# Performance work log

Measured on AMD Instinct MI355X. Metric: run time of the kernel, lower is better.

The kernel has to match this reference:

```python
import jax, jax.numpy as jnp
import numpy as np

N_NODES = 10000
N_EDGES = 50000
UNITS = 64
NUM_GAUSSIANS = 50
MIN_D, MAX_D, GAMMA = 0.0, 30.0, 10.0


def setup_inputs() -> dict:
    key = jax.random.key(0)
    ks = jax.random.split(key, 8)
    node_features = jax.random.normal(ks[0], (N_NODES, UNITS), dtype=jnp.float32)
    edge_indices = jax.random.randint(ks[1], (2, N_EDGES), 0, N_NODES, dtype=jnp.int32)
    distances = jax.random.uniform(ks[2], (N_EDGES,), dtype=jnp.float32) * MAX_D
    # filter network params (Dense(units) -> Dense(units*units)), glorot-ish scales
    W1 = jax.random.normal(ks[3], (NUM_GAUSSIANS, UNITS), dtype=jnp.float32) * 0.13
    b1 = jnp.zeros((UNITS,), dtype=jnp.float32)
    W2 = jax.random.normal(ks[4], (UNITS, UNITS * UNITS), dtype=jnp.float32) * 0.02
    b2 = jnp.zeros((UNITS * UNITS,), dtype=jnp.float32)
    # transform Dense(units, use_bias=False)
    Wt = jax.random.normal(ks[5], (UNITS, UNITS), dtype=jnp.float32) * 0.125
    return {"node_features": node_features, "edge_indices": edge_indices,
            "distances": distances, "W1": W1, "b1": b1, "W2": W2, "b2": b2, "Wt": Wt}


def reference(node_features, edge_indices, distances, W1, b1, W2, b2, Wt):
    # Gaussian basis expansion: [E, G]
    centers = jnp.linspace(MIN_D, MAX_D, NUM_GAUSSIANS, dtype=jnp.float32)
    dist_feat = jnp.exp(-GAMMA * jnp.square(distances[:, None] - centers[None, :]))
    # filter-generating network -> per-edge [E, U, U] filters
    h = dist_feat @ W1 + b1
    filters = (h @ W2 + b2).reshape(-1, UNITS, UNITS)
    # gather source node feats, linear transform, per-edge matvec
    src = node_features[edge_indices[0]]            # [E, U]
    transformed = src @ Wt                          # [E, U]
    filtered = jnp.einsum('eij,ej->ei', filters, transformed)  # [E, U]
    # scatter-sum to destination nodes
    messages = jax.ops.segment_sum(filtered, edge_indices[1], num_segments=N_NODES)
    # shifted softplus: f(0) = 0
    return jax.nn.softplus(messages) - jnp.log(jnp.float32(2.0))
```

## Files before the change

kernel.cpp:

```cpp
#include <hip/hip_runtime.h>
#include <stdint.h>

#define UNITS 64
#define UU 4096
#define NG 50
#define NSLOT 51
#define GAMMA_C 10.0f
#define STEP_C (30.0f / 49.0f)
#define NWIN 4
#define NBKT 47
#define NCHK 64

typedef __attribute__((ext_vector_type(8))) short bf16x8;
typedef __attribute__((ext_vector_type(4))) float f32x4;

union bfr_t { bf16x8 v; uint32_t u[4]; };

__device__ __forceinline__ uint16_t f2bf(float x) {
  uint32_t u = __float_as_uint(x);
  u += 0x7fffu + ((u >> 16) & 1u);
  return (uint16_t)(u >> 16);
}
__device__ __forceinline__ uint32_t pk_bf16(float lo, float hi) {
  uint32_t r;
  asm("v_cvt_pk_bf16_f32 %0, %1, %2" : "=v"(r) : "v"(lo), "v"(hi));
  return r;
}
__device__ __forceinline__ int lo_of(float d) {
  int lo = (int)floorf(d * (1.0f / STEP_C)) - 1;
  return min(max(lo, 0), NG - NWIN);
}

__global__ void __launch_bounds__(256) k_hist(const float* __restrict__ dist,
                                              int* __restrict__ binsB,
                                              int* __restrict__ eidx, int E, int ne) {
  __shared__ int hloc[NBKT];
  for (int i = threadIdx.x; i < NBKT; i += 256) hloc[i] = 0;
  __syncthreads();
  int per = (E + NCHK - 1) / NCHK;
  int e0 = blockIdx.x * per, e1 = min(e0 + per, E);
  for (int e = e0 + threadIdx.x; e < e1; e += 256)
    atomicAdd(&hloc[lo_of(dist[e])], 1);
  __syncthreads();
  for (int i = threadIdx.x; i < 64; i += 256)
    binsB[blockIdx.x * 64 + i] = (i < NBKT) ? hloc[i] : 0;
  for (int i = blockIdx.x * 256 + threadIdx.x; i < ne; i += NCHK * 256) eidx[i] = -1;
}

__global__ void __launch_bounds__(256) k_at(
    const float* __restrict__ W1, const float* __restrict__ b1,
    const float* __restrict__ W2, const float* __restrict__ b2,
    const float* __restrict__ Wt, const float* __restrict__ dist,
    uint16_t* __restrict__ T5B, float* __restrict__ msg,
    const int* __restrict__ binsB, int* __restrict__ eidx,
    int n_out, int E) {
  int g = blockIdx.y, bx = blockIdx.x;
  if (g >= NSLOT) {
    if (g < NSLOT + 8) {
      int n4 = n_out >> 2;
      float4 z = {0.f, 0.f, 0.f, 0.f};
      for (int t = ((g - NSLOT) * 16 + bx) * 256 + threadIdx.x; t < n4; t += 128 * 256)
        reinterpret_cast<float4*>(msg)[t] = z;
      return;
    }
    __shared__ int hbase[NBKT], hcur[NBKT];
    int sb = (g - (NSLOT + 8)) * 16 + bx;
    int per = (E + NCHK - 1) / NCHK;
    int e0 = sb * per, e1 = min(e0 + per, E);
    if (threadIdx.x < 64) {
      int lane = threadIdx.x;
      int tot = 0, pre = 0;
      for (int j = 0; j < NCHK; ++j) {
        int v = binsB[j * 64 + lane];
        tot += v;
        if (j < sb) pre += v;
      }
      int cap = (tot + 15) & ~15;
      int inc = cap;
      #pragma unroll
      for (int s = 1; s < 64; s <<= 1) {
        int t = __shfl_up(inc, s, 64);
        if (lane >= s) inc += t;
      }
      if (lane < NBKT) { hbase[lane] = (inc - cap) + pre; hcur[lane] = 0; }
    }
    __syncthreads();
    for (int e = e0 + threadIdx.x; e < e1; e += 256) {
      int b = lo_of(dist[e]);
      int p = hbase[b] + atomicAdd(&hcur[b], 1);
      eidx[p] = e;
    }
    return;
  }
  __shared__ float Aloc[256];
  __shared__ float WtL[64 * 65];
  const int t = threadIdx.x;
  const int ij = bx * 256 + t;

  #pragma unroll
  for (int q = 0; q < 4; ++q) {
    int idx = q * 256 + t;
    float4 v = reinterpret_cast<const float4*>(Wt)[idx];
    int mm = idx >> 4, jj = (idx & 15) * 4;
    float* dst = &WtL[mm * 65 + jj];
    dst[0] = v.x; dst[1] = v.y; dst[2] = v.z; dst[3] = v.w;
  }
  {
    float acc = 0.f;
    if (g < NG) {
      const float* w1r = W1 + g * UNITS;
      #pragma unroll 8
      for (int k = 0; k < UNITS; ++k) acc = fmaf(w1r[k], W2[k * UU + ij], acc);
    } else {
      #pragma unroll 8
      for (int k = 0; k < UNITS; ++k) acc = fmaf(b1[k], W2[k * UU + ij], acc);
      acc += b2[ij];
    }
    Aloc[t] = acc;
  }
  __syncthreads();

  const int i_local = t >> 6, m = t & 63;
  const float* ar = &Aloc[i_local * 64];
  const float* wr = &WtL[m * 65];
  float acc = 0.f;
  #pragma unroll 8
  for (int j = 0; j < UNITS; ++j) acc = fmaf(ar[j], wr[j], acc);
  const int gi = bx * 4 + i_local;
  T5B[(((g << 3) + (m >> 3)) << 9) + (gi << 3) + (m & 7)] = f2bf(acc);
}

__global__ void __launch_bounds__(256) k_em(
    const float* __restrict__ nf, const int* __restrict__ ei,
    const float* __restrict__ dist, const uint16_t* __restrict__ T5B,
    const int* __restrict__ eidx, const int* __restrict__ binsB,
    float* __restrict__ msg, int E) {
  __shared__ float tile[4][16 * 64];
  int w = threadIdx.x >> 6, l = threadIdx.x & 63;
  int lr = l & 15, lg = l >> 4;

  int tot = 0;
  #pragma unroll 8
  for (int j = 0; j < NCHK; ++j) tot += binsB[j * 64 + l];
  int tcap = (tot + 15) >> 4;
  int p = tcap;
  #pragma unroll
  for (int s = 1; s < 64; s <<= 1) {
    int tt = __shfl_up(p, s, 64);
    if (l >= s) p += tt;
  }
  int total = __shfl(p, 63);

  int tA = (blockIdx.x * 4 + w) * 2, tB = tA + 1;
  if (tA >= total) return;
  bool actB = (tB < total);

  uint64_t mA = __ballot(tA < p);
  int bA = __ffsll((unsigned long long)mA) - 1;
  int bB = bA;
  if (actB) {
    uint64_t mB = __ballot(tB < p);
    bB = __ffsll((unsigned long long)mB) - 1;
  }

  int eA = eidx[tA * 16 + lr];
  int eB = actB ? eidx[tB * 16 + lr] : -1;
  bool vA = (eA >= 0), vB = (eB >= 0);
  int srcA = vA ? ei[eA] : 0, dstA = vA ? ei[E + eA] : -1;
  int srcB = vB ? ei[eB] : 0, dstB = vB ? ei[E + eB] : -1;
  float dA = vA ? dist[eA] : 3.0e30f;
  float dB = vB ? dist[eB] : 3.0e30f;

  bfr_t afrA[2], afrB[2];
  {
    const float4* abA = reinterpret_cast<const float4*>(nf + srcA * UNITS) + lg * 2;
    const float4* abB = reinterpret_cast<const float4*>(nf + srcB * UNITS) + lg * 2;
    #pragma unroll
    for (int kk = 0; kk < 2; ++kk) {
      float4 a0 = abA[kk * 8], a1 = abA[kk * 8 + 1];
      float4 b0 = abB[kk * 8], b1 = abB[kk * 8 + 1];
      afrA[kk].u[0] = pk_bf16(a0.x, a0.y); afrA[kk].u[1] = pk_bf16(a0.z, a0.w);
      afrA[kk].u[2] = pk_bf16(a1.x, a1.y); afrA[kk].u[3] = pk_bf16(a1.z, a1.w);
      afrB[kk].u[0] = pk_bf16(b0.x, b0.y); afrB[kk].u[1] = pk_bf16(b0.z, b0.w);
      afrB[kk].u[2] = pk_bf16(b1.x, b1.y); afrB[kk].u[3] = pk_bf16(b1.z, b1.w);
    }
  }

  float* tw = tile[w];
  auto run_tile = [&](int b, float d, bool valid, int dst, bfr_t* afr) {
    float df[5];
    #pragma unroll
    for (int s = 0; s < NWIN; ++s) {
      float tt = d - (float)(b + s) * STEP_C;
      df[s] = __expf(-GAMMA_C * tt * tt);
    }
    df[NWIN] = valid ? 1.f : 0.f;

    f32x4 run[4] = {};
    #pragma unroll
    for (int s = 0; s < 5; ++s) {
      int g = (s < NWIN) ? (b + s) : NG;
      const char* bb = (const char*)T5B + (g << 13) + (lg << 10) + (lr << 6);
      f32x4 acc[4] = {};
      #pragma unroll
      for (int kk = 0; kk < 2; ++kk)
        #pragma unroll
        for (int nt = 0; nt < 4; ++nt) {
          bf16x8 bf = *reinterpret_cast<const bf16x8*>(bb + (kk << 12) + (nt << 4));
          acc[nt] = __builtin_amdgcn_mfma_f32_16x16x32_bf16(afr[kk].v, bf, acc[nt], 0, 0, 0);
        }
      float dfq[4];
      #pragma unroll
      for (int q = 0; q < 4; ++q) dfq[q] = __shfl(df[s], lg * 4 + q, 64);
      #pragma unroll
      for (int nt = 0; nt < 4; ++nt)
        #pragma unroll
        for (int q = 0; q < 4; ++q)
          run[nt][q] = fmaf(dfq[q], acc[nt][q], run[nt][q]);
    }

    #pragma unroll
    for (int q = 0; q < 4; ++q) {
      float4 v4 = {run[0][q], run[1][q], run[2][q], run[3][q]};
      *reinterpret_cast<float4*>(&tw[(lg * 4 + q) * 64 + 4 * lr]) = v4;
    }
    asm volatile("" ::: "memory");

    #pragma unroll
    for (int r = 0; r < 16; ++r) {
      int dr = __shfl(dst, r, 64);
      if (dr < 0) continue;
      atomicAdd(&msg[dr * UNITS + l], tw[r * 64 + l]);
    }
  };

  run_tile(bA, dA, vA, dstA, afrA);
  if (actB) run_tile(bB, dB, vB, dstB, afrB);
}

__global__ void k_final(const float* __restrict__ msg, float* __restrict__ out,
                        int n_out) {
  int i4 = blockIdx.x * 256 + threadIdx.x;
  if (i4 >= (n_out >> 2)) return;
  float4 a = reinterpret_cast<const float4*>(msg)[i4];
  float4 r;
  r.x = ((a.x > 0.f) ? (a.x + log1pf(__expf(-a.x))) : log1pf(__expf(a.x))) - 0.69314718056f;
  r.y = ((a.y > 0.f) ? (a.y + log1pf(__expf(-a.y))) : log1pf(__expf(a.y))) - 0.69314718056f;
  r.z = ((a.z > 0.f) ? (a.z + log1pf(__expf(-a.z))) : log1pf(__expf(a.z))) - 0.69314718056f;
  r.w = ((a.w > 0.f) ? (a.w + log1pf(__expf(-a.w))) : log1pf(__expf(a.w))) - 0.69314718056f;
  reinterpret_cast<float4*>(out)[i4] = r;
}

extern "C" void kernel_launch(void* const* d_in, const int* in_sizes, int n_in,
                              void* d_out, int out_size, void* d_ws, size_t ws_size,
                              hipStream_t stream) {
  const float* nf   = (const float*)d_in[0];
  const int*   ei   = (const int*)d_in[1];
  const float* dist = (const float*)d_in[2];
  const float* W1   = (const float*)d_in[3];
  const float* b1   = (const float*)d_in[4];
  const float* W2   = (const float*)d_in[5];
  const float* b2   = (const float*)d_in[6];
  const float* Wt   = (const float*)d_in[7];
  float* out = (float*)d_out;

  int E = in_sizes[2];
  int n_out = out_size;

  int mt = E / 16 + NBKT + 1;
  int ne = mt * 16;

  char* ws = (char*)d_ws;
  size_t off_msg   = 417792;
  size_t off_binsB = off_msg + (size_t)n_out * 4;
  size_t off_eidx  = off_binsB + NCHK * 64 * 4;

  uint16_t* T5B   = (uint16_t*)ws;
  float*    msg   = (float*)(ws + off_msg);
  int*      binsB = (int*)(ws + off_binsB);
  int*      eidx  = (int*)(ws + off_eidx);

  k_hist<<<NCHK, 256, 0, stream>>>(dist, binsB, eidx, E, ne);
  k_at  <<<dim3(16, NSLOT + 12), 256, 0, stream>>>(W1, b1, W2, b2, Wt, dist,
                                                   T5B, msg, binsB, eidx, n_out, E);
  k_em  <<<(mt + 7) / 8, 256, 0, stream>>>(nf, ei, dist, T5B, eidx, binsB, msg, E);
  k_final<<<((n_out >> 2) + 255) / 256, 256, 0, stream>>>(msg, out, n_out);
}
```

Measured before the change: 43.10 us.

## Fold histogram kernel into scatter blocks by recomputing full histogram per block

Removes the separate histogram kernel; each scatter block in k_at now recomputes the full distance-bucket histogram in shared memory and its own prefix counts, and block 0 publishes totals to a small meta array and fills only the padding slots with -1. k_em reads bucket totals directly from meta instead of summing 64 chunk rows. This saves one kernel launch and the full eidx initialization, at the cost of each of 64 blocks redundantly scanning all edge distances.

```diff
diff --git a/kernel.cpp b/kernel.cpp
--- a/kernel.cpp
+++ b/kernel.cpp
@@ -31,28 +31,12 @@
   return min(max(lo, 0), NG - NWIN);
 }
 
-__global__ void __launch_bounds__(256) k_hist(const float* __restrict__ dist,
-                                              int* __restrict__ binsB,
-                                              int* __restrict__ eidx, int E, int ne) {
-  __shared__ int hloc[NBKT];
-  for (int i = threadIdx.x; i < NBKT; i += 256) hloc[i] = 0;
-  __syncthreads();
-  int per = (E + NCHK - 1) / NCHK;
-  int e0 = blockIdx.x * per, e1 = min(e0 + per, E);
-  for (int e = e0 + threadIdx.x; e < e1; e += 256)
-    atomicAdd(&hloc[lo_of(dist[e])], 1);
-  __syncthreads();
-  for (int i = threadIdx.x; i < 64; i += 256)
-    binsB[blockIdx.x * 64 + i] = (i < NBKT) ? hloc[i] : 0;
-  for (int i = blockIdx.x * 256 + threadIdx.x; i < ne; i += NCHK * 256) eidx[i] = -1;
-}
-
 __global__ void __launch_bounds__(256) k_at(
     const float* __restrict__ W1, const float* __restrict__ b1,
     const float* __restrict__ W2, const float* __restrict__ b2,
     const float* __restrict__ Wt, const float* __restrict__ dist,
     uint16_t* __restrict__ T5B, float* __restrict__ msg,
-    const int* __restrict__ binsB, int* __restrict__ eidx,
+    int* __restrict__ meta, int* __restrict__ eidx,
     int n_out, int E) {
   int g = blockIdx.y, bx = blockIdx.x;
   if (g >= NSLOT) {
@@ -63,18 +47,23 @@
         reinterpret_cast<float4*>(msg)[t] = z;
       return;
     }
-    __shared__ int hbase[NBKT], hcur[NBKT];
+    __shared__ int htot[NBKT], hpre[NBKT], hbase[NBKT], hcur[NBKT];
     int sb = (g - (NSLOT + 8)) * 16 + bx;
     int per = (E + NCHK - 1) / NCHK;
     int e0 = sb * per, e1 = min(e0 + per, E);
+    for (int i = threadIdx.x; i < NBKT; i += 256) {
+      htot[i] = 0; hpre[i] = 0; hcur[i] = 0;
+    }
+    __syncthreads();
+    for (int e = threadIdx.x; e < E; e += 256) {
+      int b = lo_of(dist[e]);
+      atomicAdd(&htot[b], 1);
+      if (e < e0) atomicAdd(&hpre[b], 1);
+    }
+    __syncthreads();
     if (threadIdx.x < 64) {
       int lane = threadIdx.x;
-      int tot = 0, pre = 0;
-      for (int j = 0; j < NCHK; ++j) {
-        int v = binsB[j * 64 + lane];
-        tot += v;
-        if (j < sb) pre += v;
-      }
+      int tot = (lane < NBKT) ? htot[lane] : 0;
       int cap = (tot + 15) & ~15;
       int inc = cap;
       #pragma unroll
@@ -82,13 +71,23 @@
         int t = __shfl_up(inc, s, 64);
         if (lane >= s) inc += t;
       }
-      if (lane < NBKT) { hbase[lane] = (inc - cap) + pre; hcur[lane] = 0; }
+      if (lane < NBKT) hbase[lane] = (inc - cap) + hpre[lane];
     }
     __syncthreads();
     for (int e = e0 + threadIdx.x; e < e1; e += 256) {
       int b = lo_of(dist[e]);
       int p = hbase[b] + atomicAdd(&hcur[b], 1);
       eidx[p] = e;
+    }
+    if (sb == 0) {
+      if (threadIdx.x < 64)
+        meta[threadIdx.x] = (threadIdx.x < NBKT) ? htot[threadIdx.x] : 0;
+      if (threadIdx.x < NBKT) {
+        int b0 = hbase[threadIdx.x];
+        int t = htot[threadIdx.x];
+        int c = (t + 15) & ~15;
+        for (int i = b0 + t; i < b0 + c; ++i) eidx[i] = -1;
+      }
     }
     return;
   }
@@ -133,15 +132,13 @@
 __global__ void __launch_bounds__(256) k_em(
     const float* __restrict__ nf, const int* __restrict__ ei,
     const float* __restrict__ dist, const uint16_t* __restrict__ T5B,
-    const int* __restrict__ eidx, const int* __restrict__ binsB,
+    const int* __restrict__ eidx, const int* __restrict__ meta,
     float* __restrict__ msg, int E) {
   __shared__ float tile[4][16 * 64];
   int w = threadIdx.x >> 6, l = threadIdx.x & 63;
   int lr = l & 15, lg = l >> 4;
 
-  int tot = 0;
-  #pragma unroll 8
-  for (int j = 0; j < NCHK; ++j) tot += binsB[j * 64 + l];
+  int tot = (l < NBKT) ? meta[l] : 0;
   int tcap = (tot + 15) >> 4;
   int p = tcap;
   #pragma unroll
@@ -268,21 +265,19 @@
   int n_out = out_size;
 
   int mt = E / 16 + NBKT + 1;
-  int ne = mt * 16;
 
   char* ws = (char*)d_ws;
-  size_t off_msg   = 417792;
-  size_t off_binsB = off_msg + (size_t)n_out * 4;
-  size_t off_eidx  = off_binsB + NCHK * 64 * 4;
-
-  uint16_t* T5B   = (uint16_t*)ws;
-  float*    msg   = (float*)(ws + off_msg);
-  int*      binsB = (int*)(ws + off_binsB);
-  int*      eidx  = (int*)(ws + off_eidx);
-
-  k_hist<<<NCHK, 256, 0, stream>>>(dist, binsB, eidx, E, ne);
+  size_t off_msg  = 417792;
+  size_t off_meta = off_msg + (size_t)n_out * 4;
+  size_t off_eidx = off_meta + 64 * 4;
+
+  uint16_t* T5B  = (uint16_t*)ws;
+  float*    msg  = (float*)(ws + off_msg);
+  int*      meta = (int*)(ws + off_meta);
+  int*      eidx = (int*)(ws + off_eidx);
+
   k_at  <<<dim3(16, NSLOT + 12), 256, 0, stream>>>(W1, b1, W2, b2, Wt, dist,
-                                                   T5B, msg, binsB, eidx, n_out, E);
-  k_em  <<<(mt + 7) / 8, 256, 0, stream>>>(nf, ei, dist, T5B, eidx, binsB, msg, E);
+                                                   T5B, msg, meta, eidx, n_out, E);
+  k_em  <<<(mt + 7) / 8, 256, 0, stream>>>(nf, ei, dist, T5B, eidx, meta, msg, E);
   k_final<<<((n_out >> 2) + 255) / 256, 256, 0, stream>>>(msg, out, n_out);
 }
```

Measured after the change: 64.89 us. 1.51x slower.
